# Performance work log

Hardware: AMD Instinct MI355X
Metric: run time of the kernel (lower is better)

The kernel has to match this reference:

```python
import jax, jax.numpy as jnp
import numpy as np

N_NODES = 50000
N_EDGES = 600000
D = 128


def setup_inputs() -> dict:
    key = jax.random.key(0)
    ks = jax.random.split(key, 8)
    x = jax.random.normal(ks[0], (N_NODES, D), dtype=jnp.float32)
    edge_index = jax.random.randint(ks[1], (2, N_EDGES), 0, N_NODES, dtype=jnp.int64)
    s = 1.0 / np.sqrt(D)
    W_l1 = jax.random.uniform(ks[2], (D, D), jnp.float32, -s, s)
    W_r1 = jax.random.uniform(ks[3], (D, D), jnp.float32, -s, s)
    b1 = jnp.zeros((D,), jnp.float32)
    W_l2 = jax.random.uniform(ks[4], (D, D), jnp.float32, -s, s)
    W_r2 = jax.random.uniform(ks[5], (D, D), jnp.float32, -s, s)
    b2 = jnp.zeros((D,), jnp.float32)
    return {"x": x, "edge_index": edge_index, "W_l1": W_l1, "W_r1": W_r1,
            "b1": b1, "W_l2": W_l2, "W_r2": W_r2, "b2": b2}


def _sage_conv(x, src, dst, W_l, W_r, b):
    # mean aggregation over incoming edges (src -> dst), PyG SAGEConv semantics
    n = x.shape[0]
    msg = x[src]                                               # [E, D] gather
    agg = jax.ops.segment_sum(msg, dst, num_segments=n)        # [N, D] scatter-add
    cnt = jax.ops.segment_sum(jnp.ones((src.shape[0],), x.dtype), dst, num_segments=n)
    mean = agg / jnp.maximum(cnt, 1.0)[:, None]
    return mean @ W_l + x @ W_r + b


def reference(x, edge_index, W_l1, W_r1, b1, W_l2, W_r2, b2):
    src, dst = edge_index[0], edge_index[1]
    h = jax.nn.relu(_sage_conv(x, src, dst, W_l1, W_r1, b1))
    out = _sage_conv(h, src, dst, W_l2, W_r2, b2)
    return out
```

## Files before the change

kernel.cpp:

```cpp
#include <hip/hip_runtime.h>
#include <hip/hip_bf16.h>

#define N_NODES 50000
#define N_EDGES 600000
#define D 128
#define K2 256
#define MAXDEG 64

#define BUILD_BLOCKS ((N_EDGES / 4 + 255) / 256)
#define CVT_BLOCKS   (N_NODES * 16 / 256)
#define PREPW_BLOCKS (2 * D * K2 / 256)
#define PREP_GRID (BUILD_BLOCKS + CVT_BLOCKS + PREPW_BLOCKS)

typedef __bf16 bf16x8 __attribute__((ext_vector_type(8)));
typedef float  f32x16 __attribute__((ext_vector_type(16)));

__device__ __forceinline__ unsigned short f32_to_bf16_rne(float f) {
    unsigned int u = __builtin_bit_cast(unsigned int, f);
    unsigned int r = (u + 0x7fffu + ((u >> 16) & 1u)) >> 16;
    return (unsigned short)r;
}
__device__ __forceinline__ unsigned pk2(float lo, float hi) {
    return (unsigned)f32_to_bf16_rne(lo) | ((unsigned)f32_to_bf16_rne(hi) << 16);
}
__device__ __forceinline__ float bfl(unsigned int u) { return __builtin_bit_cast(float, u << 16); }
__device__ __forceinline__ float bfh(unsigned int u) { return __builtin_bit_cast(float, u & 0xffff0000u); }

__global__ __launch_bounds__(256) void prep_kernel(
    const float* __restrict__ x, const int* __restrict__ ei,
    const float* __restrict__ Wl1, const float* __restrict__ Wr1,
    const float* __restrict__ Wl2, const float* __restrict__ Wr2,
    unsigned short* __restrict__ A0, unsigned short* __restrict__ WT,
    int* __restrict__ counts, int* __restrict__ slots)
{
    const int b = blockIdx.x;
    if (b < BUILD_BLOCKS) {
        int e4 = (b * 256 + threadIdx.x) * 4;
        if (e4 < N_EDGES) {
            int4 s4 = *(const int4*)(ei + e4);
            int4 d4 = *(const int4*)(ei + N_EDGES + e4);
            int p0 = atomicAdd(&counts[d4.x], 1);
            int p1 = atomicAdd(&counts[d4.y], 1);
            int p2 = atomicAdd(&counts[d4.z], 1);
            int p3 = atomicAdd(&counts[d4.w], 1);
            if (p0 < MAXDEG) slots[(size_t)d4.x * MAXDEG + p0] = s4.x;
            if (p1 < MAXDEG) slots[(size_t)d4.y * MAXDEG + p1] = s4.y;
            if (p2 < MAXDEG) slots[(size_t)d4.z * MAXDEG + p2] = s4.z;
            if (p3 < MAXDEG) slots[(size_t)d4.w * MAXDEG + p3] = s4.w;
        }
    } else if (b < BUILD_BLOCKS + CVT_BLOCKS) {
        int idx = (b - BUILD_BLOCKS) * 256 + threadIdx.x;
        int node = idx >> 4, g = idx & 15;
        const float4* xp = (const float4*)(x + (size_t)node * D + g * 8);
        float4 v0 = xp[0], v1 = xp[1];
        uint4 o;
        o.x = pk2(v0.x, v0.y); o.y = pk2(v0.z, v0.w);
        o.z = pk2(v1.x, v1.y); o.w = pk2(v1.z, v1.w);
        ((uint4*)A0)[(size_t)node * 16 + g] = o;
    } else {
        int idx = (b - BUILD_BLOCKS - CVT_BLOCKS) * 256 + threadIdx.x;
        int layer = idx >> 15, rem = idx & 32767;
        int n = rem >> 8, k = rem & 255;
        const float* Wl = layer ? Wl2 : Wl1;
        const float* Wr = layer ? Wr2 : Wr1;
        float v = (k < D) ? Wl[k * D + n] : Wr[(k - D) * D + n];
        WT[((size_t)layer << 15) + n * K2 + k] = f32_to_bf16_rne(v);
    }
}

template <bool RELU, bool OUT_BF16>
__global__ __launch_bounds__(256) void layer_kernel(
    const unsigned short* __restrict__ Xin,
    const int* __restrict__ counts, const int* __restrict__ slots,
    const unsigned short* __restrict__ WT,
    const float* __restrict__ bias,
    unsigned short* __restrict__ Hout,
    float* __restrict__ outf)
{
    __shared__ uint4 As4[32 * 33];
    const int tid = threadIdx.x;
    const int lane = tid & 63;
    const int wv = tid >> 6;
    const int base = blockIdx.x * 32;
    const int g = lane >> 4;
    const int u = lane & 15;
    const uint4* X4 = (const uint4*)Xin;
    const int nodeb = base + wv * 8;

    const int n0 = nodeb + g;
    const int n1 = nodeb + 4 + g;
    const bool ok0 = n0 < N_NODES, ok1 = n1 < N_NODES;

    int cnt0 = 0, cnt1 = 0;
    if (ok0) cnt0 = counts[n0];
    if (ok1) cnt1 = counts[n1];

    int sreg[2][4];
    #pragma unroll
    for (int r = 0; r < 4; ++r) {
        sreg[0][r] = ok0 ? slots[(size_t)n0 * MAXDEG + r * 16 + u] : 0;
        sreg[1][r] = ok1 ? slots[(size_t)n1 * MAXDEG + r * 16 + u] : 0;
    }

    uint4 xv0 = {0u,0u,0u,0u}, xv1 = {0u,0u,0u,0u};
    if (ok0) xv0 = X4[(size_t)n0 * 16 + u];
    if (ok1) xv1 = X4[(size_t)n1 * 16 + u];

    cnt0 = cnt0 > MAXDEG ? MAXDEG : cnt0;
    cnt1 = cnt1 > MAXDEG ? MAXDEG : cnt1;

    #pragma unroll
    for (int s = 0; s < 2; ++s) {
        const int m = wv * 8 + s * 4 + g;
        const int cnt = s ? cnt1 : cnt0;
        float a0 = 0.f, a1 = 0.f, a2 = 0.f, a3 = 0.f;
        float a4 = 0.f, a5 = 0.f, a6 = 0.f, a7 = 0.f;

        #pragma unroll
        for (int e = 0; e < 16; ++e) {
            int idx = __shfl(sreg[s][0], g * 16 + e, 64);
            if (e < cnt) {
                uint4 v = X4[(size_t)idx * 16 + u];
                a0 += bfl(v.x); a1 += bfh(v.x); a2 += bfl(v.y); a3 += bfh(v.y);
                a4 += bfl(v.z); a5 += bfh(v.z); a6 += bfl(v.w); a7 += bfh(v.w);
            }
        }
        #pragma unroll
        for (int r = 1; r < 4; ++r) {
            if (__any(cnt > r * 16)) {
                #pragma unroll
                for (int e = 0; e < 16; ++e) {
                    int idx = __shfl(sreg[s][r], g * 16 + e, 64);
                    if (r * 16 + e < cnt) {
                        uint4 v = X4[(size_t)idx * 16 + u];
                        a0 += bfl(v.x); a1 += bfh(v.x); a2 += bfl(v.y); a3 += bfh(v.y);
                        a4 += bfl(v.z); a5 += bfh(v.z); a6 += bfl(v.w); a7 += bfh(v.w);
                    }
                }
            }
        }

        const float inv = 1.0f / fmaxf((float)cnt, 1.0f);
        uint4 o;
        o.x = pk2(a0 * inv, a1 * inv); o.y = pk2(a2 * inv, a3 * inv);
        o.z = pk2(a4 * inv, a5 * inv); o.w = pk2(a6 * inv, a7 * inv);
        As4[u * 33 + m] = o;
    }

    As4[(16 + u) * 33 + (wv * 8 + g)]     = xv0;
    As4[(16 + u) * 33 + (wv * 8 + 4 + g)] = xv1;

    __syncthreads();

    const int m = lane & 31;
    const int kg = lane >> 5;
    const int col = wv * 32 + m;
    const uint4* bp = (const uint4*)(WT + (size_t)col * K2 + kg * 8);
    const bf16x8* afrag = (const bf16x8*)As4;

    f32x16 acc = {};
    #pragma unroll
    for (int s = 0; s < 16; ++s) {
        bf16x8 a = afrag[(s * 2 + kg) * 33 + m];
        bf16x8 b = __builtin_bit_cast(bf16x8, bp[s * 2]);
        acc = __builtin_amdgcn_mfma_f32_32x32x16_bf16(a, b, acc, 0, 0, 0);
    }

    const float bc = bias[col];
    const int halfadd = kg * 4;
    #pragma unroll
    for (int r = 0; r < 16; ++r) {
        int rw = base + (r & 3) + 8 * (r >> 2) + halfadd;
        if (rw < N_NODES) {
            float v = acc[r] + bc;
            if (RELU) v = fmaxf(v, 0.0f);
            if (OUT_BF16) Hout[(size_t)rw * D + col] = f32_to_bf16_rne(v);
            else outf[(size_t)rw * D + col] = v;
        }
    }
}

extern "C" void kernel_launch(void* const* d_in, const int* in_sizes, int n_in,
                              void* d_out, int out_size, void* d_ws, size_t ws_size,
                              hipStream_t stream) {
    const float* x   = (const float*)d_in[0];
    const int*   ei  = (const int*)d_in[1];
    const float* Wl1 = (const float*)d_in[2];
    const float* Wr1 = (const float*)d_in[3];
    const float* b1  = (const float*)d_in[4];
    const float* Wl2 = (const float*)d_in[5];
    const float* Wr2 = (const float*)d_in[6];
    const float* b2  = (const float*)d_in[7];
    float* out = (float*)d_out;

    unsigned short* A0 = (unsigned short*)d_ws;
    unsigned short* A1 = A0 + (size_t)N_NODES * D;
    unsigned short* WT = A1 + (size_t)N_NODES * D;
    int* counts = (int*)(WT + 2 * D * K2);
    int* slots  = counts + N_NODES;

    const int layerBlocks = (N_NODES + 31) / 32;

    hipMemsetAsync(counts, 0, N_NODES * sizeof(int), stream);
    prep_kernel<<<PREP_GRID, 256, 0, stream>>>(x, ei, Wl1, Wr1, Wl2, Wr2, A0, WT, counts, slots);

    layer_kernel<true, true><<<layerBlocks, 256, 0, stream>>>(
        A0, counts, slots, WT, b1, A1, nullptr);
    layer_kernel<false, false><<<layerBlocks, 256, 0, stream>>>(
        A1, counts, slots, WT + (size_t)D * K2, b2, nullptr, out);
}
```

Measured before the change: 230.9 us.

## Batch neighbor gathers, merge edge build into convert blocks, set occupancy bound

```diff
diff --git a/kernel.cpp b/kernel.cpp
--- a/kernel.cpp
+++ b/kernel.cpp
@@ -7,10 +7,9 @@
 #define K2 256
 #define MAXDEG 64
 
-#define BUILD_BLOCKS ((N_EDGES / 4 + 255) / 256)
 #define CVT_BLOCKS   (N_NODES * 16 / 256)
 #define PREPW_BLOCKS (2 * D * K2 / 256)
-#define PREP_GRID (BUILD_BLOCKS + CVT_BLOCKS + PREPW_BLOCKS)
+#define PREP_GRID (CVT_BLOCKS + PREPW_BLOCKS)
 
 typedef __bf16 bf16x8 __attribute__((ext_vector_type(8)));
 typedef float  f32x16 __attribute__((ext_vector_type(16)));
@@ -34,11 +33,19 @@
     int* __restrict__ counts, int* __restrict__ slots)
 {
     const int b = blockIdx.x;
-    if (b < BUILD_BLOCKS) {
-        int e4 = (b * 256 + threadIdx.x) * 4;
-        if (e4 < N_EDGES) {
-            int4 s4 = *(const int4*)(ei + e4);
-            int4 d4 = *(const int4*)(ei + N_EDGES + e4);
+    if (b < CVT_BLOCKS) {
+        int idx = b * 256 + threadIdx.x;
+        int e4 = idx * 4;
+        int4 s4 = {0,0,0,0}, d4 = {0,0,0,0};
+        const bool doE = e4 < N_EDGES;
+        if (doE) {
+            s4 = *(const int4*)(ei + e4);
+            d4 = *(const int4*)(ei + N_EDGES + e4);
+        }
+        int node = idx >> 4, g = idx & 15;
+        const float4* xp = (const float4*)(x + (size_t)node * D + g * 8);
+        float4 v0 = xp[0], v1 = xp[1];
+        if (doE) {
             int p0 = atomicAdd(&counts[d4.x], 1);
             int p1 = atomicAdd(&counts[d4.y], 1);
             int p2 = atomicAdd(&counts[d4.z], 1);
@@ -48,17 +55,12 @@
             if (p2 < MAXDEG) slots[(size_t)d4.z * MAXDEG + p2] = s4.z;
             if (p3 < MAXDEG) slots[(size_t)d4.w * MAXDEG + p3] = s4.w;
         }
-    } else if (b < BUILD_BLOCKS + CVT_BLOCKS) {
-        int idx = (b - BUILD_BLOCKS) * 256 + threadIdx.x;
-        int node = idx >> 4, g = idx & 15;
-        const float4* xp = (const float4*)(x + (size_t)node * D + g * 8);
-        float4 v0 = xp[0], v1 = xp[1];
         uint4 o;
         o.x = pk2(v0.x, v0.y); o.y = pk2(v0.z, v0.w);
         o.z = pk2(v1.x, v1.y); o.w = pk2(v1.z, v1.w);
         ((uint4*)A0)[(size_t)node * 16 + g] = o;
     } else {
-        int idx = (b - BUILD_BLOCKS - CVT_BLOCKS) * 256 + threadIdx.x;
+        int idx = (b - CVT_BLOCKS) * 256 + threadIdx.x;
         int layer = idx >> 15, rem = idx & 32767;
         int n = rem >> 8, k = rem & 255;
         const float* Wl = layer ? Wl2 : Wl1;
@@ -69,7 +71,7 @@
 }
 
 template <bool RELU, bool OUT_BF16>
-__global__ __launch_bounds__(256) void layer_kernel(
+__global__ __launch_bounds__(256, 4) void layer_kernel(
     const unsigned short* __restrict__ Xin,
     const int* __restrict__ counts, const int* __restrict__ slots,
     const unsigned short* __restrict__ WT,
@@ -117,24 +119,25 @@
         float a4 = 0.f, a5 = 0.f, a6 = 0.f, a7 = 0.f;
 
         #pragma unroll
-        for (int e = 0; e < 16; ++e) {
-            int idx = __shfl(sreg[s][0], g * 16 + e, 64);
-            if (e < cnt) {
-                uint4 v = X4[(size_t)idx * 16 + u];
-                a0 += bfl(v.x); a1 += bfh(v.x); a2 += bfl(v.y); a3 += bfh(v.y);
-                a4 += bfl(v.z); a5 += bfh(v.z); a6 += bfl(v.w); a7 += bfh(v.w);
-            }
-        }
-        #pragma unroll
-        for (int r = 1; r < 4; ++r) {
-            if (__any(cnt > r * 16)) {
+        for (int r = 0; r < 4; ++r) {
+            if (r == 0 || __any(cnt > r * 16)) {
+                int idxv[16];
                 #pragma unroll
                 for (int e = 0; e < 16; ++e) {
-                    int idx = __shfl(sreg[s][r], g * 16 + e, 64);
+                    int t = __shfl(sreg[s][r], g * 16 + e, 64);
+                    idxv[e] = (r * 16 + e < cnt) ? t : 0;
+                }
+                uint4 vv[16];
+                #pragma unroll
+                for (int e = 0; e < 16; ++e)
+                    vv[e] = X4[(size_t)idxv[e] * 16 + u];
+                #pragma unroll
+                for (int e = 0; e < 16; ++e) {
                     if (r * 16 + e < cnt) {
-                        uint4 v = X4[(size_t)idx * 16 + u];
-                        a0 += bfl(v.x); a1 += bfh(v.x); a2 += bfl(v.y); a3 += bfh(v.y);
-                        a4 += bfl(v.z); a5 += bfh(v.z); a6 += bfl(v.w); a7 += bfh(v.w);
+                        a0 += bfl(vv[e].x); a1 += bfh(vv[e].x);
+                        a2 += bfl(vv[e].y); a3 += bfh(vv[e].y);
+                        a4 += bfl(vv[e].z); a5 += bfh(vv[e].z);
+                        a6 += bfl(vv[e].w); a7 += bfh(vv[e].w);
                     }
                 }
             }
```

After: 202.5 us. -12.3%, faster.
